# Kernel tuning notes

Hardware: AMD Instinct MI355X
Metric: run time of the kernel (lower is better)

The kernel has to match this reference:

```python
import jax, jax.numpy as jnp
import numpy as np

LN_EPS = 1e-5


def setup_inputs() -> dict:
    key = jax.random.key(0)
    ks = jax.random.split(key, 6)
    B, M, N, D = 16, 128, 128, 128
    NM, H = 16, 512
    xav = float(np.sqrt(2.0 / (D + D)))  # xavier_normal over (in_dim, out_dim) fan
    return {
        "x": jax.random.normal(ks[0], (B, M, N, D), jnp.float32),
        "w1": jax.random.normal(ks[1], (D, D, NM, 2), jnp.float32) * xav,
        "w2": jax.random.normal(ks[2], (D, D, NM, 2), jnp.float32) * xav,
        "ff_w0": jax.random.normal(ks[3], (D, H), jnp.float32) * float(1.0 / np.sqrt(D)),
        "ff_b0": jnp.zeros((H,), jnp.float32),
        "ff_w1": jax.random.normal(ks[4], (H, D), jnp.float32) * float(1.0 / np.sqrt(H)),
        "ff_b1": jnp.zeros((D,), jnp.float32),
        "ln_g": jnp.ones((D,), jnp.float32),
        "ln_b": jnp.zeros((D,), jnp.float32),
    }


def _layer_norm(h, g, b):
    mu = jnp.mean(h, axis=-1, keepdims=True)
    var = jnp.mean(jnp.square(h - mu), axis=-1, keepdims=True)
    return (h - mu) * jax.lax.rsqrt(var + LN_EPS) * g + b


def _forward_fourier(x, w1, w2):
    # x: [B, M, N, I] -> [B, I, M, N]
    xt = jnp.transpose(x, (0, 3, 1, 2))
    B, I, M, N = xt.shape
    nm = w1.shape[2]
    cw1 = w1[..., 0] + 1j * w1[..., 1]  # [I, O, nm]
    cw2 = w2[..., 0] + 1j * w2[..., 1]
    O = cw1.shape[1]

    # Fourier along last axis (y)
    fty = jnp.fft.rfft(xt, axis=-1, norm="ortho")                    # [B,I,M,N//2+1]
    f1 = jnp.einsum("bixy,ioy->boxy", fty[..., :nm], cw1)            # [B,O,M,nm]
    pad_y = jnp.zeros((B, O, M, N // 2 + 1 - nm), dtype=f1.dtype)
    xy = jnp.fft.irfft(jnp.concatenate([f1, pad_y], axis=-1), n=N, axis=-1, norm="ortho")

    # Fourier along second-to-last axis (x)
    ftx = jnp.fft.rfft(xt, axis=-2, norm="ortho")                    # [B,I,M//2+1,N]
    f2 = jnp.einsum("bixy,iox->boxy", ftx[:, :, :nm, :], cw2)        # [B,O,nm,N]
    pad_x = jnp.zeros((B, O, M // 2 + 1 - nm, N), dtype=f2.dtype)
    xx = jnp.fft.irfft(jnp.concatenate([f2, pad_x], axis=-2), n=M, axis=-2, norm="ortho")

    return jnp.transpose(xx + xy, (0, 2, 3, 1))  # [B,M,N,O]


def reference(x, w1, w2, ff_w0, ff_b0, ff_w1, ff_b1, ln_g, ln_b):
    h = _forward_fourier(x, w1, w2)
    # backcast FeedForward: Linear -> ReLU -> Linear -> LayerNorm (dropout=0)
    h1 = jax.nn.relu(jnp.einsum("bmni,ih->bmnh", h, ff_w0) + ff_b0)
    h2 = jnp.einsum("bmnh,ho->bmno", h1, ff_w1) + ff_b1
    return _layer_norm(h2, ln_g, ln_b)
```

## Files before the change

kernel.cpp:

```cpp
#include <hip/hip_runtime.h>


#define LN_EPS 1e-5f
#define NMODES 16
#define FROW 4096
#define HROW 16384

typedef __attribute__((ext_vector_type(8))) short short8;
typedef __attribute__((ext_vector_type(4))) short short4v;
typedef __attribute__((ext_vector_type(4))) float f32x4;

__device__ __forceinline__ ushort f2bf(float f) {
    unsigned u = __float_as_uint(f);
    unsigned r = (u + 0x7FFFu + ((u >> 16) & 1u)) >> 16;
    return (ushort)r;
}
__device__ __forceinline__ float bf2f(ushort h) {
    return __uint_as_float(((unsigned)h) << 16);
}

__global__ void k_setup(float* __restrict__ Tc, float* __restrict__ Ts,
                        float* __restrict__ IT) {
    const float invs = 0.08838834764831845f;
    for (int idx = threadIdx.x; idx < NMODES * 128; idx += blockDim.x) {
        int k = idx >> 7, n = idx & 127;
        int p = (k * n) & 127;
        float th = (float)p * (6.283185307179586f / 128.0f);
        float c = cosf(th), s = sinf(th);
        Tc[idx] = c * invs;
        Ts[idx] = -s * invs;
        float ck = (k == 0) ? invs : 2.0f * invs;
        IT[n * 32 + 2 * k]     = ck * c;
        IT[n * 32 + 2 * k + 1] = -ck * s;
    }
}

__global__ void k_wpack(const float* __restrict__ w, ushort* __restrict__ Wph,
                        ushort* __restrict__ Wpl) {
    int idx = blockIdx.x * 256 + threadIdx.x;
    int k  = idx >> 16;
    int op = (idx >> 8) & 255;
    int ip = idx & 255;
    int i = ip & 127, o = op & 127;
    const float* base = w + (((i << 7) | o) * NMODES + k) * 2;
    float re = base[0], im = base[1];
    float v = (ip < 128) ? ((op < 128) ? re : im)
                         : ((op < 128) ? -im : re);
    ushort hi = f2bf(v);
    ushort lo = f2bf(v - bf2f(hi));
    Wph[idx] = hi;
    Wpl[idx] = lo;
}

__global__ __launch_bounds__(256) void k_wcvt(const float* __restrict__ w0,
        const float* __restrict__ w1, ushort* __restrict__ w0t,
        ushort* __restrict__ w1t) {
    int idx = blockIdx.x * 256 + threadIdx.x;
    int h = idx >> 7, k = idx & 127;
    w0t[idx] = f2bf(w0[k * 512 + h]);
    int o = idx >> 9, hh = idx & 511;
    w1t[idx] = f2bf(w1[hh * 128 + o]);
}

__global__ __launch_bounds__(128) void k_fft(const float* __restrict__ x,
        const float* __restrict__ Tc, const float* __restrict__ Ts,
        float* __restrict__ F, int mode) {
    __shared__ float Tc_s[NMODES * 128];
    __shared__ float Ts_s[NMODES * 128];
    for (int e = threadIdx.x; e < NMODES * 128; e += 128) {
        Tc_s[e] = Tc[e];
        Ts_s[e] = Ts[e];
    }
    __syncthreads();
    int row = blockIdx.x;
    int base, ts;
    if (mode == 0) { base = row * HROW; ts = 128; }
    else { base = (row >> 7) * 2097152 + (row & 127) * 128; ts = 16384; }
    int i = threadIdx.x;
    float re[NMODES], im[NMODES];
#pragma unroll
    for (int k = 0; k < NMODES; ++k) { re[k] = 0.f; im[k] = 0.f; }
    for (int tb = 0; tb < 32; ++tb) {
        int t0 = tb * 4;
        float xv0 = x[base + (t0 + 0) * ts + i];
        float xv1 = x[base + (t0 + 1) * ts + i];
        float xv2 = x[base + (t0 + 2) * ts + i];
        float xv3 = x[base + (t0 + 3) * ts + i];
#pragma unroll
        for (int k = 0; k < NMODES; ++k) {
            f32x4 c4 = *(const f32x4*)&Tc_s[k * 128 + t0];
            f32x4 s4 = *(const f32x4*)&Ts_s[k * 128 + t0];
            re[k] += xv0 * c4[0] + xv1 * c4[1] + xv2 * c4[2] + xv3 * c4[3];
            im[k] += xv0 * s4[0] + xv1 * s4[1] + xv2 * s4[2] + xv3 * s4[3];
        }
    }
    float* outp = F + row * FROW;
#pragma unroll
    for (int k = 0; k < NMODES; ++k) {
        outp[k * 256 + i]       = re[k];
        outp[k * 256 + 128 + i] = im[k];
    }
}

__global__ __launch_bounds__(256) void k_mixm(const float* __restrict__ A,
        const ushort* __restrict__ Wph, const ushort* __restrict__ Wpl,
        float* __restrict__ outF) {
    __shared__ ushort Ah[32 * 264];
    __shared__ ushort Al[32 * 264];
    int tid = threadIdx.x;
    int kt = blockIdx.x & 15;
    int bm0 = (blockIdx.x >> 4) * 32;
    {
        int row = tid >> 3, cg = tid & 7;
        const float* arow = A + (bm0 + row) * FROW + kt * 256 + cg * 32;
        ushort* ah = &Ah[row * 264 + cg * 32];
        ushort* al = &Al[row * 264 + cg * 32];
#pragma unroll
        for (int j = 0; j < 8; ++j) {
            f32x4 v = *(const f32x4*)(arow + j * 4);
            short4v h4, l4;
#pragma unroll
            for (int q = 0; q < 4; ++q) {
                ushort h = f2bf(v[q]);
                h4[q] = (short)h;
                l4[q] = (short)f2bf(v[q] - bf2f(h));
            }
            *(short4v*)(ah + j * 4) = h4;
            *(short4v*)(al + j * 4) = l4;
        }
    }
    __syncthreads();
    int lane = tid & 63, wid = tid >> 6;
    int frow = lane & 15, fk8 = (lane >> 4) * 8, fr4 = (lane >> 4) * 4;
    f32x4 acc[2][4];
#pragma unroll
    for (int a = 0; a < 2; ++a)
#pragma unroll
        for (int c = 0; c < 4; ++c) acc[a][c] = {0.f, 0.f, 0.f, 0.f};
    const ushort* wph = Wph + kt * 65536;
    const ushort* wpl = Wpl + kt * 65536;
#pragma unroll
    for (int kk = 0; kk < 8; ++kk) {
        short8 ah0 = *(const short8*)&Ah[(frow)      * 264 + kk * 32 + fk8];
        short8 ah1 = *(const short8*)&Ah[(16 + frow) * 264 + kk * 32 + fk8];
        short8 al0 = *(const short8*)&Al[(frow)      * 264 + kk * 32 + fk8];
        short8 al1 = *(const short8*)&Al[(16 + frow) * 264 + kk * 32 + fk8];
#pragma unroll
        for (int tc = 0; tc < 4; ++tc) {
            int op = wid * 64 + tc * 16 + frow;
            int base = op * 256 + kk * 32 + fk8;
            short8 wh = *(const short8*)&wph[base];
            short8 wl = *(const short8*)&wpl[base];
            acc[0][tc] = __builtin_amdgcn_mfma_f32_16x16x32_bf16(ah0, wh, acc[0][tc], 0, 0, 0);
            acc[0][tc] = __builtin_amdgcn_mfma_f32_16x16x32_bf16(ah0, wl, acc[0][tc], 0, 0, 0);
            acc[0][tc] = __builtin_amdgcn_mfma_f32_16x16x32_bf16(al0, wh, acc[0][tc], 0, 0, 0);
            acc[1][tc] = __builtin_amdgcn_mfma_f32_16x16x32_bf16(ah1, wh, acc[1][tc], 0, 0, 0);
            acc[1][tc] = __builtin_amdgcn_mfma_f32_16x16x32_bf16(ah1, wl, acc[1][tc], 0, 0, 0);
            acc[1][tc] = __builtin_amdgcn_mfma_f32_16x16x32_bf16(al1, wh, acc[1][tc], 0, 0, 0);
        }
    }
#pragma unroll
    for (int tr = 0; tr < 2; ++tr)
#pragma unroll
        for (int tc = 0; tc < 4; ++tc)
#pragma unroll
            for (int r = 0; r < 4; ++r)
                outF[(bm0 + tr * 16 + fr4 + r) * FROW + kt * 256 + wid * 64 + tc * 16 + frow]
                    = acc[tr][tc][r];
}

__global__ __launch_bounds__(256) void k_icdft(const float* __restrict__ f,
        const float* __restrict__ IT, float* __restrict__ h, int mode) {
    __shared__ float IT_s[128 * 32];
    __shared__ float f_s[32 * 128];
    int row = blockIdx.x;
    for (int e = threadIdx.x; e < 4096; e += 256) {
        IT_s[e] = IT[e];
        f_s[e]  = f[row * FROW + e];
    }
    __syncthreads();
    int o = threadIdx.x & 127, nh = threadIdx.x >> 7;
    int outbase, ostride;
    if (mode == 0) { outbase = row * HROW + o; ostride = 128; }
    else { outbase = (row >> 7) * 2097152 + (row & 127) * 128 + o; ostride = 16384; }
    for (int nb = 0; nb < 8; ++nb) {
        int n0 = nh * 64 + nb * 8;
        float acc[8];
#pragma unroll
        for (int j = 0; j < 8; ++j) acc[j] = 0.f;
#pragma unroll
        for (int kpb = 0; kpb < 8; ++kpb) {
            int kp0 = kpb * 4;
            float f0 = f_s[kp0 * 128 + o];
            float f1v = f_s[kp0 * 128 + 128 + o];
            float f2v = f_s[kp0 * 128 + 256 + o];
            float f3v = f_s[kp0 * 128 + 384 + o];
#pragma unroll
            for (int j = 0; j < 8; ++j) {
                f32x4 it = *(const f32x4*)&IT_s[(n0 + j) * 32 + kp0];
                acc[j] += f0 * it[0] + f1v * it[1] + f2v * it[2] + f3v * it[3];
            }
        }
        if (mode == 0) {
#pragma unroll
            for (int j = 0; j < 8; ++j) h[outbase + (n0 + j) * ostride] = acc[j];
        } else {
#pragma unroll
            for (int j = 0; j < 8; ++j) h[outbase + (n0 + j) * ostride] += acc[j];
        }
    }
}

__global__ __launch_bounds__(256) void k_ffn(float* __restrict__ hio,
        const ushort* __restrict__ w0t, const float* __restrict__ b0,
        const ushort* __restrict__ w1t, const float* __restrict__ b1,
        const float* __restrict__ g, const float* __restrict__ bb) {
    __shared__ __align__(16) ushort h1_s[64 * 136];
    __shared__ float b0_s[512];
    __shared__ float gb_s[256];
    __shared__ float b1_s[128];
    __shared__ float ps_s[64 * 4];
    __shared__ float pq_s[64 * 4];
    __shared__ float mr_s[64 * 2];

    int tid = threadIdx.x;
    int R0 = blockIdx.x * 64;
    for (int e = tid; e < 512; e += 256) b0_s[e] = b0[e];
    if (tid < 128) {
        gb_s[tid] = g[tid];
        gb_s[128 + tid] = bb[tid];
        b1_s[tid] = b1[tid];
    }

    int lane = tid & 63, wid = tid >> 6;
    int frow = lane & 15;
    int fk8 = (lane >> 4) * 8;
    int fr4 = (lane >> 4) * 4;

    short8 a1f[4][4];
#pragma unroll
    for (int tr = 0; tr < 4; ++tr)
#pragma unroll
        for (int kk = 0; kk < 4; ++kk) {
            const float* src = &hio[(R0 + tr * 16 + frow) * 128 + kk * 32 + fk8];
            f32x4 v0 = *(const f32x4*)src;
            f32x4 v1 = *(const f32x4*)(src + 4);
            short8 t;
#pragma unroll
            for (int j = 0; j < 4; ++j) {
                t[j]     = (short)f2bf(v0[j]);
                t[4 + j] = (short)f2bf(v1[j]);
            }
            a1f[tr][kk] = t;
        }

    f32x4 acc2[4][2];
#pragma unroll
    for (int a = 0; a < 4; ++a)
#pragma unroll
        for (int c = 0; c < 2; ++c) acc2[a][c] = {0.f, 0.f, 0.f, 0.f};

    for (int hc = 0; hc < 4; ++hc) {
        __syncthreads();
#pragma unroll
        for (int tc = 0; tc < 2; ++tc) {
            int lcol = wid * 32 + tc * 16 + frow;
            int hcol = hc * 128 + lcol;
            short8 bfr[4];
#pragma unroll
            for (int kk = 0; kk < 4; ++kk)
                bfr[kk] = *(const short8*)&w0t[hcol * 128 + kk * 32 + fk8];
            f32x4 acc1[4];
#pragma unroll
            for (int a = 0; a < 4; ++a) acc1[a] = {0.f, 0.f, 0.f, 0.f};
#pragma unroll
            for (int kk = 0; kk < 4; ++kk)
#pragma unroll
                for (int tr = 0; tr < 4; ++tr)
                    acc1[tr] = __builtin_amdgcn_mfma_f32_16x16x32_bf16(
                        a1f[tr][kk], bfr[kk], acc1[tr], 0, 0, 0);
            float b0v = b0_s[hcol];
#pragma unroll
            for (int tr = 0; tr < 4; ++tr)
#pragma unroll
                for (int r = 0; r < 4; ++r) {
                    float v = acc1[tr][r] + b0v;
                    h1_s[(tr * 16 + fr4 + r) * 136 + lcol] = f2bf(fmaxf(v, 0.f));
                }
        }
        __syncthreads();
#pragma unroll
        for (int kk = 0; kk < 4; ++kk) {
            short8 a2[4];
#pragma unroll
            for (int tr = 0; tr < 4; ++tr)
                a2[tr] = *(const short8*)&h1_s[(tr * 16 + frow) * 136 + kk * 32 + fk8];
#pragma unroll
            for (int tc = 0; tc < 2; ++tc) {
                int ocol = wid * 32 + tc * 16 + frow;
                short8 b2 = *(const short8*)&w1t[ocol * 512 + hc * 128 + kk * 32 + fk8];
#pragma unroll
                for (int tr = 0; tr < 4; ++tr)
                    acc2[tr][tc] = __builtin_amdgcn_mfma_f32_16x16x32_bf16(
                        a2[tr], b2, acc2[tr][tc], 0, 0, 0);
            }
        }
    }
    float b1v0 = b1_s[wid * 32 + frow];
    float b1v1 = b1_s[wid * 32 + 16 + frow];
#pragma unroll
    for (int tr = 0; tr < 4; ++tr)
#pragma unroll
        for (int r = 0; r < 4; ++r) {
            float v0 = acc2[tr][0][r] + b1v0;
            float v1 = acc2[tr][1][r] + b1v1;
            acc2[tr][0][r] = v0;
            acc2[tr][1][r] = v1;
            float s = v0 + v1;
            float q = v0 * v0 + v1 * v1;
            s += __shfl_xor(s, 1); q += __shfl_xor(q, 1);
            s += __shfl_xor(s, 2); q += __shfl_xor(q, 2);
            s += __shfl_xor(s, 4); q += __shfl_xor(q, 4);
            s += __shfl_xor(s, 8); q += __shfl_xor(q, 8);
            if (frow == 0) {
                int row_l = tr * 16 + fr4 + r;
                ps_s[row_l * 4 + wid] = s;
                pq_s[row_l * 4 + wid] = q;
            }
        }
    __syncthreads();
    if (tid < 64) {
        float S = ps_s[tid * 4] + ps_s[tid * 4 + 1] + ps_s[tid * 4 + 2] + ps_s[tid * 4 + 3];
        float Q = pq_s[tid * 4] + pq_s[tid * 4 + 1] + pq_s[tid * 4 + 2] + pq_s[tid * 4 + 3];
        float mu = S * (1.0f / 128.0f);
        float var = Q * (1.0f / 128.0f) - mu * mu;
        mr_s[tid * 2] = mu;
        mr_s[tid * 2 + 1] = rsqrtf(fmaxf(var, 0.f) + LN_EPS);
    }
    __syncthreads();
    float g0 = gb_s[wid * 32 + frow],       bb0 = gb_s[128 + wid * 32 + frow];
    float g1 = gb_s[wid * 32 + 16 + frow],  bb1 = gb_s[128 + wid * 32 + 16 + frow];
#pragma unroll
    for (int tr = 0; tr < 4; ++tr)
#pragma unroll
        for (int r = 0; r < 4; ++r) {
            int row_l = tr * 16 + fr4 + r;
            float mu = mr_s[row_l * 2], rs = mr_s[row_l * 2 + 1];
            float* orow = &hio[(R0 + row_l) * 128 + wid * 32];
            orow[frow]      = (acc2[tr][0][r] - mu) * rs * g0 + bb0;
            orow[16 + frow] = (acc2[tr][1][r] - mu) * rs * g1 + bb1;
        }
}

extern "C" void kernel_launch(void* const* d_in, const int* in_sizes, int n_in,
                              void* d_out, int out_size, void* d_ws, size_t ws_size,
                              hipStream_t stream) {
    (void)in_sizes; (void)n_in; (void)out_size; (void)ws_size;
    const float* x   = (const float*)d_in[0];
    const float* w1  = (const float*)d_in[1];
    const float* w2  = (const float*)d_in[2];
    const float* fw0 = (const float*)d_in[3];
    const float* fb0 = (const float*)d_in[4];
    const float* fw1 = (const float*)d_in[5];
    const float* fb1 = (const float*)d_in[6];
    const float* lng = (const float*)d_in[7];
    const float* lnb = (const float*)d_in[8];
    float* out = (float*)d_out;

    char* ws = (char*)d_ws;
    float*  Tc  = (float*)(ws);
    float*  Ts  = (float*)(ws + 8192);
    float*  IT  = (float*)(ws + 16384);
    ushort* Wph = (ushort*)(ws + 32768);
    ushort* Wpl = (ushort*)(ws + 32768 + 2097152);
    ushort* w0t = (ushort*)(ws + 4227072);
    ushort* w1t = (ushort*)(ws + 4358144);
    float*  buf0 = (float*)(ws + 4489216);
    float*  buf1 = (float*)(ws + 4489216 + 33554432);

    k_setup<<<1, 256, 0, stream>>>(Tc, Ts, IT);
    k_wcvt <<<256, 256, 0, stream>>>(fw0, fw1, w0t, w1t);

    k_wpack<<<4096, 256, 0, stream>>>(w1, Wph, Wpl);
    k_fft  <<<2048, 128, 0, stream>>>(x, Tc, Ts, buf0, 0);
    k_mixm <<<1024, 256, 0, stream>>>(buf0, Wph, Wpl, buf1);
    k_icdft<<<2048, 256, 0, stream>>>(buf1, IT, out, 0);

    k_wpack<<<4096, 256, 0, stream>>>(w2, Wph, Wpl);
    k_fft  <<<2048, 128, 0, stream>>>(x, Tc, Ts, buf0, 1);
    k_mixm <<<1024, 256, 0, stream>>>(buf0, Wph, Wpl, buf1);
    k_icdft<<<2048, 256, 0, stream>>>(buf1, IT, out, 1);

    k_ffn<<<4096, 256, 0, stream>>>(out, w0t, fb0, w1t, fb1, lng, lnb);
}
```

Baseline: 564.0 us.

## Emit bf16 intermediate from inverse DFT and stage FFN tiles through LDS

The second inverse-DFT pass now writes the summed spectral output as bf16 into a separate workspace buffer when the workspace is large enough, halving the bytes the FFN kernel reads. The FFN kernel loads its input tile cooperatively into LDS with coalesced vector loads instead of per-lane strided register fragments. It also stages the LayerNorm output through LDS for coalesced vector stores. This trades higher LDS usage (lower occupancy risk) and a gated path that depends on workspace size for less global traffic and better coalescing.

```diff
diff --git a/kernel.cpp b/kernel.cpp
--- a/kernel.cpp
+++ b/kernel.cpp
@@ -7,6 +7,7 @@
 #define HROW 16384
 
 typedef __attribute__((ext_vector_type(8))) short short8;
+typedef __attribute__((ext_vector_type(8))) ushort ushort8;
 typedef __attribute__((ext_vector_type(4))) short short4v;
 typedef __attribute__((ext_vector_type(4))) float f32x4;
 
@@ -170,7 +171,8 @@
 }
 
 __global__ __launch_bounds__(256) void k_icdft(const float* __restrict__ f,
-        const float* __restrict__ IT, float* __restrict__ h, int mode) {
+        const float* __restrict__ IT, float* __restrict__ h,
+        ushort* __restrict__ hbf, int mode, int use_bf) {
     __shared__ float IT_s[128 * 32];
     __shared__ float f_s[32 * 128];
     int row = blockIdx.x;
@@ -204,6 +206,12 @@
         if (mode == 0) {
 #pragma unroll
             for (int j = 0; j < 8; ++j) h[outbase + (n0 + j) * ostride] = acc[j];
+        } else if (use_bf) {
+#pragma unroll
+            for (int j = 0; j < 8; ++j) {
+                int ix = outbase + (n0 + j) * ostride;
+                hbf[ix] = f2bf(h[ix] + acc[j]);
+            }
         } else {
 #pragma unroll
             for (int j = 0; j < 8; ++j) h[outbase + (n0 + j) * ostride] += acc[j];
@@ -211,48 +219,49 @@
     }
 }
 
-__global__ __launch_bounds__(256) void k_ffn(float* __restrict__ hio,
+__global__ __launch_bounds__(256) void k_ffn(const ushort* __restrict__ hbf,
+        const float* __restrict__ h32, float* __restrict__ out,
         const ushort* __restrict__ w0t, const float* __restrict__ b0,
         const ushort* __restrict__ w1t, const float* __restrict__ b1,
-        const float* __restrict__ g, const float* __restrict__ bb) {
-    __shared__ __align__(16) ushort h1_s[64 * 136];
-    __shared__ float b0_s[512];
+        const float* __restrict__ g, const float* __restrict__ bb, int use_bf) {
+    __shared__ __align__(16) char smem[34816];
+    ushort* h_s  = (ushort*)smem;
+    ushort* h1_s = (ushort*)(smem + 17408);
+    float*  h2f  = (float*)smem;
+    float*  ps_s = (float*)(smem + 33792);
+    __shared__ float b0q_s[512];
     __shared__ float gb_s[256];
     __shared__ float b1_s[128];
-    __shared__ float ps_s[64 * 4];
-    __shared__ float pq_s[64 * 4];
-    __shared__ float mr_s[64 * 2];
+    __shared__ float mr_s[128];
 
     int tid = threadIdx.x;
     int R0 = blockIdx.x * 64;
-    for (int e = tid; e < 512; e += 256) b0_s[e] = b0[e];
-    if (tid < 128) {
-        gb_s[tid] = g[tid];
-        gb_s[128 + tid] = bb[tid];
-        b1_s[tid] = b1[tid];
-    }
+    {
+        int srow = tid >> 2, scol = (tid & 3) * 32;
+        if (use_bf) {
+            const ushort* src = hbf + (R0 + srow) * 128 + scol;
+#pragma unroll
+            for (int j = 0; j < 4; ++j)
+                *(ushort8*)&h_s[srow * 136 + scol + j * 8] = *(const ushort8*)(src + j * 8);
+        } else {
+            const float* src = h32 + (R0 + srow) * 128 + scol;
+#pragma unroll
+            for (int j = 0; j < 4; ++j) {
+                f32x4 v0 = *(const f32x4*)(src + j * 8);
+                f32x4 v1 = *(const f32x4*)(src + j * 8 + 4);
+                ushort8 t;
+#pragma unroll
+                for (int q = 0; q < 4; ++q) { t[q] = f2bf(v0[q]); t[4 + q] = f2bf(v1[q]); }
+                *(ushort8*)&h_s[srow * 136 + scol + j * 8] = t;
+            }
+        }
+    }
+    for (int e = tid; e < 512; e += 256) b0q_s[e] = b0[e];
+    if (tid < 128) { gb_s[tid] = g[tid]; gb_s[128 + tid] = bb[tid]; b1_s[tid] = b1[tid]; }
+    __syncthreads();
 
     int lane = tid & 63, wid = tid >> 6;
-    int frow = lane & 15;
-    int fk8 = (lane >> 4) * 8;
-    int fr4 = (lane >> 4) * 4;
-
-    short8 a1f[4][4];
-#pragma unroll
-    for (int tr = 0; tr < 4; ++tr)
-#pragma unroll
-        for (int kk = 0; kk < 4; ++kk) {
-            const float* src = &hio[(R0 + tr * 16 + frow) * 128 + kk * 32 + fk8];
-            f32x4 v0 = *(const f32x4*)src;
-            f32x4 v1 = *(const f32x4*)(src + 4);
-            short8 t;
-#pragma unroll
-            for (int j = 0; j < 4; ++j) {
-                t[j]     = (short)f2bf(v0[j]);
-                t[4 + j] = (short)f2bf(v1[j]);
-            }
-            a1f[tr][kk] = t;
-        }
+    int frow = lane & 15, fk8 = (lane >> 4) * 8, fr4 = (lane >> 4) * 4;
 
     f32x4 acc2[4][2];
 #pragma unroll
@@ -261,7 +270,6 @@
         for (int c = 0; c < 2; ++c) acc2[a][c] = {0.f, 0.f, 0.f, 0.f};
 
     for (int hc = 0; hc < 4; ++hc) {
-        __syncthreads();
 #pragma unroll
         for (int tc = 0; tc < 2; ++tc) {
             int lcol = wid * 32 + tc * 16 + frow;
@@ -276,10 +284,12 @@
 #pragma unroll
             for (int kk = 0; kk < 4; ++kk)
 #pragma unroll
-                for (int tr = 0; tr < 4; ++tr)
+                for (int tr = 0; tr < 4; ++tr) {
+                    short8 av = *(const short8*)&h_s[(tr * 16 + frow) * 136 + kk * 32 + fk8];
                     acc1[tr] = __builtin_amdgcn_mfma_f32_16x16x32_bf16(
-                        a1f[tr][kk], bfr[kk], acc1[tr], 0, 0, 0);
-            float b0v = b0_s[hcol];
+                        av, bfr[kk], acc1[tr], 0, 0, 0);
+                }
+            float b0v = b0q_s[hcol];
 #pragma unroll
             for (int tr = 0; tr < 4; ++tr)
 #pragma unroll
@@ -290,22 +300,25 @@
         }
         __syncthreads();
 #pragma unroll
-        for (int kk = 0; kk < 4; ++kk) {
-            short8 a2[4];
-#pragma unroll
-            for (int tr = 0; tr < 4; ++tr)
-                a2[tr] = *(const short8*)&h1_s[(tr * 16 + frow) * 136 + kk * 32 + fk8];
-#pragma unroll
-            for (int tc = 0; tc < 2; ++tc) {
-                int ocol = wid * 32 + tc * 16 + frow;
-                short8 b2 = *(const short8*)&w1t[ocol * 512 + hc * 128 + kk * 32 + fk8];
-#pragma unroll
-                for (int tr = 0; tr < 4; ++tr)
+        for (int tc = 0; tc < 2; ++tc) {
+            int ocol = wid * 32 + tc * 16 + frow;
+            short8 b2f[4];
+#pragma unroll
+            for (int kk = 0; kk < 4; ++kk)
+                b2f[kk] = *(const short8*)&w1t[ocol * 512 + hc * 128 + kk * 32 + fk8];
+#pragma unroll
+            for (int kk = 0; kk < 4; ++kk)
+#pragma unroll
+                for (int tr = 0; tr < 4; ++tr) {
+                    short8 a2 = *(const short8*)&h1_s[(tr * 16 + frow) * 136 + kk * 32 + fk8];
                     acc2[tr][tc] = __builtin_amdgcn_mfma_f32_16x16x32_bf16(
-                        a2[tr], b2, acc2[tr][tc], 0, 0, 0);
-            }
-        }
-    }
+                        a2, b2f[kk], acc2[tr][tc], 0, 0, 0);
+                }
+        }
+        __syncthreads();
+    }
+
+    float* pq_s = b0q_s;
     float b1v0 = b1_s[wid * 32 + frow];
     float b1v1 = b1_s[wid * 32 + 16 + frow];
 #pragma unroll
@@ -334,28 +347,35 @@
         float Q = pq_s[tid * 4] + pq_s[tid * 4 + 1] + pq_s[tid * 4 + 2] + pq_s[tid * 4 + 3];
         float mu = S * (1.0f / 128.0f);
         float var = Q * (1.0f / 128.0f) - mu * mu;
-        mr_s[tid * 2] = mu;
-        mr_s[tid * 2 + 1] = rsqrtf(fmaxf(var, 0.f) + LN_EPS);
-    }
-    __syncthreads();
-    float g0 = gb_s[wid * 32 + frow],       bb0 = gb_s[128 + wid * 32 + frow];
-    float g1 = gb_s[wid * 32 + 16 + frow],  bb1 = gb_s[128 + wid * 32 + 16 + frow];
+        mr_s[tid] = mu;
+        mr_s[64 + tid] = rsqrtf(fmaxf(var, 0.f) + LN_EPS);
+    }
+    __syncthreads();
+    float g0 = gb_s[wid * 32 + frow],      c0 = gb_s[128 + wid * 32 + frow];
+    float g1 = gb_s[wid * 32 + 16 + frow], c1 = gb_s[128 + wid * 32 + 16 + frow];
 #pragma unroll
     for (int tr = 0; tr < 4; ++tr)
 #pragma unroll
         for (int r = 0; r < 4; ++r) {
             int row_l = tr * 16 + fr4 + r;
-            float mu = mr_s[row_l * 2], rs = mr_s[row_l * 2 + 1];
-            float* orow = &hio[(R0 + row_l) * 128 + wid * 32];
-            orow[frow]      = (acc2[tr][0][r] - mu) * rs * g0 + bb0;
-            orow[16 + frow] = (acc2[tr][1][r] - mu) * rs * g1 + bb1;
-        }
+            float mu = mr_s[row_l], rs = mr_s[64 + row_l];
+            h2f[row_l * 132 + wid * 32 + frow]      = (acc2[tr][0][r] - mu) * rs * g0 + c0;
+            h2f[row_l * 132 + wid * 32 + 16 + frow] = (acc2[tr][1][r] - mu) * rs * g1 + c1;
+        }
+    __syncthreads();
+    {
+        int srow = tid >> 2, scol = (tid & 3) * 32;
+        float* dst = out + (R0 + srow) * 128 + scol;
+#pragma unroll
+        for (int j = 0; j < 8; ++j)
+            *(f32x4*)(dst + j * 4) = *(const f32x4*)&h2f[srow * 132 + scol + j * 4];
+    }
 }
 
 extern "C" void kernel_launch(void* const* d_in, const int* in_sizes, int n_in,
                               void* d_out, int out_size, void* d_ws, size_t ws_size,
                               hipStream_t stream) {
-    (void)in_sizes; (void)n_in; (void)out_size; (void)ws_size;
+    (void)in_sizes; (void)n_in; (void)out_size;
     const float* x   = (const float*)d_in[0];
     const float* w1  = (const float*)d_in[1];
     const float* w2  = (const float*)d_in[2];
@@ -377,6 +397,9 @@
     ushort* w1t = (ushort*)(ws + 4358144);
     float*  buf0 = (float*)(ws + 4489216);
     float*  buf1 = (float*)(ws + 4489216 + 33554432);
+    ushort* hbf  = (ushort*)(ws + 71598080);
+    const size_t need = 71598080ull + 67108864ull;
+    int use_bf = (ws_size >= need) ? 1 : 0;
 
     k_setup<<<1, 256, 0, stream>>>(Tc, Ts, IT);
     k_wcvt <<<256, 256, 0, stream>>>(fw0, fw1, w0t, w1t);
@@ -384,12 +407,12 @@
     k_wpack<<<4096, 256, 0, stream>>>(w1, Wph, Wpl);
     k_fft  <<<2048, 128, 0, stream>>>(x, Tc, Ts, buf0, 0);
     k_mixm <<<1024, 256, 0, stream>>>(buf0, Wph, Wpl, buf1);
-    k_icdft<<<2048, 256, 0, stream>>>(buf1, IT, out, 0);
+    k_icdft<<<2048, 256, 0, stream>>>(buf1, IT, out, hbf, 0, use_bf);
 
     k_wpack<<<4096, 256, 0, stream>>>(w2, Wph, Wpl);
     k_fft  <<<2048, 128, 0, stream>>>(x, Tc, Ts, buf0, 1);
     k_mixm <<<1024, 256, 0, stream>>>(buf0, Wph, Wpl, buf1);
-    k_icdft<<<2048, 256, 0, stream>>>(buf1, IT, out, 1);
-
-    k_ffn<<<4096, 256, 0, stream>>>(out, w0t, fb0, w1t, fb1, lng, lnb);
-}
+    k_icdft<<<2048, 256, 0, stream>>>(buf1, IT, out, hbf, 1, use_bf);
+
+    k_ffn<<<4096, 256, 0, stream>>>(hbf, out, out, w0t, fb0, w1t, fb1, lng, lnb, use_bf);
+}
```

Result: faster. 531.3 us (-5.8%).

## Store Fourier branch outputs as bf16 and fuse their sum into FFN

Applied to the files above, without the earlier changes.

The inverse DFT now writes each branch's output as bf16 into separate contiguous buffers, avoiding the strided fp32 read-modify-write accumulation into the output. The FFN kernel reads both bf16 buffers, adds them in shared memory and applies the full FFN plus LayerNorm, using one wave per 64-row block that holds all 128 output columns. This lets LayerNorm finish within a wave without block-level reductions or extra barriers. It also runs k_mixm in place on buf0, and falls back to an fp32 path when the workspace is too small. The risks are extra bf16 rounding of the branch outputs and heavier register pressure in the single-wave FFN.

```diff
diff --git a/kernel.cpp b/kernel.cpp
--- a/kernel.cpp
+++ b/kernel.cpp
@@ -7,6 +7,7 @@
 #define HROW 16384
 
 typedef __attribute__((ext_vector_type(8))) short short8;
+typedef __attribute__((ext_vector_type(8))) ushort ushort8;
 typedef __attribute__((ext_vector_type(4))) short short4v;
 typedef __attribute__((ext_vector_type(4))) float f32x4;
 
@@ -170,7 +171,8 @@
 }
 
 __global__ __launch_bounds__(256) void k_icdft(const float* __restrict__ f,
-        const float* __restrict__ IT, float* __restrict__ h, int mode) {
+        const float* __restrict__ IT, ushort* __restrict__ obf,
+        float* __restrict__ h32, ushort* __restrict__ hbfs, int mode) {
     __shared__ float IT_s[128 * 32];
     __shared__ float f_s[32 * 128];
     int row = blockIdx.x;
@@ -180,9 +182,6 @@
     }
     __syncthreads();
     int o = threadIdx.x & 127, nh = threadIdx.x >> 7;
-    int outbase, ostride;
-    if (mode == 0) { outbase = row * HROW + o; ostride = 128; }
-    else { outbase = (row >> 7) * 2097152 + (row & 127) * 128 + o; ostride = 16384; }
     for (int nb = 0; nb < 8; ++nb) {
         int n0 = nh * 64 + nb * 8;
         float acc[8];
@@ -203,159 +202,145 @@
         }
         if (mode == 0) {
 #pragma unroll
-            for (int j = 0; j < 8; ++j) h[outbase + (n0 + j) * ostride] = acc[j];
+            for (int j = 0; j < 8; ++j)
+                obf[row * HROW + (n0 + j) * 128 + o] = f2bf(acc[j]);
+        } else if (mode == 1) {
+#pragma unroll
+            for (int j = 0; j < 8; ++j)
+                h32[row * HROW + (n0 + j) * 128 + o] = acc[j];
         } else {
 #pragma unroll
-            for (int j = 0; j < 8; ++j) h[outbase + (n0 + j) * ostride] += acc[j];
-        }
-    }
-}
-
-__global__ __launch_bounds__(256) void k_ffn(float* __restrict__ hio,
+            for (int j = 0; j < 8; ++j) {
+                int ix = (row >> 7) * 2097152 + (row & 127) * 128 + o + (n0 + j) * 16384;
+                hbfs[ix] = f2bf(h32[ix] + acc[j]);
+            }
+        }
+    }
+}
+
+__global__ __launch_bounds__(64, 2) void k_ffn(const ushort* __restrict__ hy,
+        const ushort* __restrict__ hx, const ushort* __restrict__ hbfs,
+        float* __restrict__ out,
         const ushort* __restrict__ w0t, const float* __restrict__ b0,
         const ushort* __restrict__ w1t, const float* __restrict__ b1,
-        const float* __restrict__ g, const float* __restrict__ bb) {
-    __shared__ __align__(16) ushort h1_s[64 * 136];
-    __shared__ float b0_s[512];
-    __shared__ float gb_s[256];
-    __shared__ float b1_s[128];
-    __shared__ float ps_s[64 * 4];
-    __shared__ float pq_s[64 * 4];
-    __shared__ float mr_s[64 * 2];
-
-    int tid = threadIdx.x;
+        const float* __restrict__ g, const float* __restrict__ bb, int two) {
+    __shared__ __align__(16) ushort h_s[64 * 136];
+    __shared__ __align__(16) ushort h1_s[64 * 40];
+    int lane = threadIdx.x;
     int R0 = blockIdx.x * 64;
-    for (int e = tid; e < 512; e += 256) b0_s[e] = b0[e];
-    if (tid < 128) {
-        gb_s[tid] = g[tid];
-        gb_s[128 + tid] = bb[tid];
-        b1_s[tid] = b1[tid];
-    }
-
-    int lane = tid & 63, wid = tid >> 6;
-    int frow = lane & 15;
-    int fk8 = (lane >> 4) * 8;
-    int fr4 = (lane >> 4) * 4;
-
-    short8 a1f[4][4];
+
+    if (two) {
+        int b = R0 >> 14, m = (R0 >> 7) & 127, n0 = R0 & 127;
+        const ushort* hyp = hy + (size_t)R0 * 128;
+        const ushort* hxp = hx + (size_t)b * 2097152 + (size_t)n0 * 16384 + m * 128;
+        for (int e = lane; e < 1024; e += 64) {
+            int rl = e >> 4, c8 = (e & 15) * 8;
+            ushort8 a = *(const ushort8*)&hyp[rl * 128 + c8];
+            ushort8 c = *(const ushort8*)&hxp[rl * 16384 + c8];
+            ushort8 t;
+#pragma unroll
+            for (int j = 0; j < 8; ++j) t[j] = f2bf(bf2f(a[j]) + bf2f(c[j]));
+            *(ushort8*)&h_s[rl * 136 + c8] = t;
+        }
+    } else {
+        for (int e = lane; e < 1024; e += 64) {
+            int rl = e >> 4, c8 = (e & 15) * 8;
+            *(ushort8*)&h_s[rl * 136 + c8] =
+                *(const ushort8*)&hbfs[(size_t)(R0 + rl) * 128 + c8];
+        }
+    }
+    __syncthreads();
+
+    int frow = lane & 15, qg = lane >> 4;
+    int fk8 = qg * 8, fr4 = qg * 4;
+
+    f32x4 acc2[4][8];
+#pragma unroll
+    for (int a = 0; a < 4; ++a)
+#pragma unroll
+        for (int c = 0; c < 8; ++c) acc2[a][c] = {0.f, 0.f, 0.f, 0.f};
+
+    for (int ch = 0; ch < 16; ++ch) {
+        short8 bfr[2][4];
+#pragma unroll
+        for (int tc2 = 0; tc2 < 2; ++tc2)
+#pragma unroll
+            for (int kk = 0; kk < 4; ++kk)
+                bfr[tc2][kk] = *(const short8*)&w0t[(ch * 32 + tc2 * 16 + frow) * 128 + kk * 32 + fk8];
+        f32x4 acc1[4][2];
+#pragma unroll
+        for (int a = 0; a < 4; ++a)
+#pragma unroll
+            for (int c = 0; c < 2; ++c) acc1[a][c] = {0.f, 0.f, 0.f, 0.f};
+#pragma unroll
+        for (int kk = 0; kk < 4; ++kk)
+#pragma unroll
+            for (int tr = 0; tr < 4; ++tr) {
+                short8 av = *(const short8*)&h_s[(tr * 16 + frow) * 136 + kk * 32 + fk8];
+#pragma unroll
+                for (int tc2 = 0; tc2 < 2; ++tc2)
+                    acc1[tr][tc2] = __builtin_amdgcn_mfma_f32_16x16x32_bf16(
+                        av, bfr[tc2][kk], acc1[tr][tc2], 0, 0, 0);
+            }
+#pragma unroll
+        for (int tc2 = 0; tc2 < 2; ++tc2) {
+            float b0v = b0[ch * 32 + tc2 * 16 + frow];
+#pragma unroll
+            for (int tr = 0; tr < 4; ++tr)
+#pragma unroll
+                for (int r = 0; r < 4; ++r)
+                    h1_s[(tr * 16 + fr4 + r) * 40 + tc2 * 16 + frow] =
+                        f2bf(fmaxf(acc1[tr][tc2][r] + b0v, 0.f));
+        }
+        short8 b2[8];
+#pragma unroll
+        for (int tc = 0; tc < 8; ++tc)
+            b2[tc] = *(const short8*)&w1t[(tc * 16 + frow) * 512 + ch * 32 + fk8];
+#pragma unroll
+        for (int tr = 0; tr < 4; ++tr) {
+            short8 a2 = *(const short8*)&h1_s[(tr * 16 + frow) * 40 + fk8];
+#pragma unroll
+            for (int tc = 0; tc < 8; ++tc)
+                acc2[tr][tc] = __builtin_amdgcn_mfma_f32_16x16x32_bf16(
+                    a2, b2[tc], acc2[tr][tc], 0, 0, 0);
+        }
+    }
+
+    float b1v[8], gv[8], bv[8];
+#pragma unroll
+    for (int tc = 0; tc < 8; ++tc) {
+        int o = tc * 16 + frow;
+        b1v[tc] = b1[o]; gv[tc] = g[o]; bv[tc] = bb[o];
+    }
 #pragma unroll
     for (int tr = 0; tr < 4; ++tr)
 #pragma unroll
-        for (int kk = 0; kk < 4; ++kk) {
-            const float* src = &hio[(R0 + tr * 16 + frow) * 128 + kk * 32 + fk8];
-            f32x4 v0 = *(const f32x4*)src;
-            f32x4 v1 = *(const f32x4*)(src + 4);
-            short8 t;
-#pragma unroll
-            for (int j = 0; j < 4; ++j) {
-                t[j]     = (short)f2bf(v0[j]);
-                t[4 + j] = (short)f2bf(v1[j]);
-            }
-            a1f[tr][kk] = t;
-        }
-
-    f32x4 acc2[4][2];
-#pragma unroll
-    for (int a = 0; a < 4; ++a)
-#pragma unroll
-        for (int c = 0; c < 2; ++c) acc2[a][c] = {0.f, 0.f, 0.f, 0.f};
-
-    for (int hc = 0; hc < 4; ++hc) {
-        __syncthreads();
-#pragma unroll
-        for (int tc = 0; tc < 2; ++tc) {
-            int lcol = wid * 32 + tc * 16 + frow;
-            int hcol = hc * 128 + lcol;
-            short8 bfr[4];
-#pragma unroll
-            for (int kk = 0; kk < 4; ++kk)
-                bfr[kk] = *(const short8*)&w0t[hcol * 128 + kk * 32 + fk8];
-            f32x4 acc1[4];
-#pragma unroll
-            for (int a = 0; a < 4; ++a) acc1[a] = {0.f, 0.f, 0.f, 0.f};
-#pragma unroll
-            for (int kk = 0; kk < 4; ++kk)
-#pragma unroll
-                for (int tr = 0; tr < 4; ++tr)
-                    acc1[tr] = __builtin_amdgcn_mfma_f32_16x16x32_bf16(
-                        a1f[tr][kk], bfr[kk], acc1[tr], 0, 0, 0);
-            float b0v = b0_s[hcol];
-#pragma unroll
-            for (int tr = 0; tr < 4; ++tr)
-#pragma unroll
-                for (int r = 0; r < 4; ++r) {
-                    float v = acc1[tr][r] + b0v;
-                    h1_s[(tr * 16 + fr4 + r) * 136 + lcol] = f2bf(fmaxf(v, 0.f));
-                }
-        }
-        __syncthreads();
-#pragma unroll
-        for (int kk = 0; kk < 4; ++kk) {
-            short8 a2[4];
-#pragma unroll
-            for (int tr = 0; tr < 4; ++tr)
-                a2[tr] = *(const short8*)&h1_s[(tr * 16 + frow) * 136 + kk * 32 + fk8];
-#pragma unroll
-            for (int tc = 0; tc < 2; ++tc) {
-                int ocol = wid * 32 + tc * 16 + frow;
-                short8 b2 = *(const short8*)&w1t[ocol * 512 + hc * 128 + kk * 32 + fk8];
-#pragma unroll
-                for (int tr = 0; tr < 4; ++tr)
-                    acc2[tr][tc] = __builtin_amdgcn_mfma_f32_16x16x32_bf16(
-                        a2[tr], b2, acc2[tr][tc], 0, 0, 0);
-            }
-        }
-    }
-    float b1v0 = b1_s[wid * 32 + frow];
-    float b1v1 = b1_s[wid * 32 + 16 + frow];
-#pragma unroll
-    for (int tr = 0; tr < 4; ++tr)
-#pragma unroll
         for (int r = 0; r < 4; ++r) {
-            float v0 = acc2[tr][0][r] + b1v0;
-            float v1 = acc2[tr][1][r] + b1v1;
-            acc2[tr][0][r] = v0;
-            acc2[tr][1][r] = v1;
-            float s = v0 + v1;
-            float q = v0 * v0 + v1 * v1;
-            s += __shfl_xor(s, 1); q += __shfl_xor(q, 1);
-            s += __shfl_xor(s, 2); q += __shfl_xor(q, 2);
-            s += __shfl_xor(s, 4); q += __shfl_xor(q, 4);
-            s += __shfl_xor(s, 8); q += __shfl_xor(q, 8);
-            if (frow == 0) {
-                int row_l = tr * 16 + fr4 + r;
-                ps_s[row_l * 4 + wid] = s;
-                pq_s[row_l * 4 + wid] = q;
-            }
-        }
-    __syncthreads();
-    if (tid < 64) {
-        float S = ps_s[tid * 4] + ps_s[tid * 4 + 1] + ps_s[tid * 4 + 2] + ps_s[tid * 4 + 3];
-        float Q = pq_s[tid * 4] + pq_s[tid * 4 + 1] + pq_s[tid * 4 + 2] + pq_s[tid * 4 + 3];
-        float mu = S * (1.0f / 128.0f);
-        float var = Q * (1.0f / 128.0f) - mu * mu;
-        mr_s[tid * 2] = mu;
-        mr_s[tid * 2 + 1] = rsqrtf(fmaxf(var, 0.f) + LN_EPS);
-    }
-    __syncthreads();
-    float g0 = gb_s[wid * 32 + frow],       bb0 = gb_s[128 + wid * 32 + frow];
-    float g1 = gb_s[wid * 32 + 16 + frow],  bb1 = gb_s[128 + wid * 32 + 16 + frow];
-#pragma unroll
-    for (int tr = 0; tr < 4; ++tr)
-#pragma unroll
-        for (int r = 0; r < 4; ++r) {
-            int row_l = tr * 16 + fr4 + r;
-            float mu = mr_s[row_l * 2], rs = mr_s[row_l * 2 + 1];
-            float* orow = &hio[(R0 + row_l) * 128 + wid * 32];
-            orow[frow]      = (acc2[tr][0][r] - mu) * rs * g0 + bb0;
-            orow[16 + frow] = (acc2[tr][1][r] - mu) * rs * g1 + bb1;
+            float s = 0.f, qq = 0.f;
+#pragma unroll
+            for (int tc = 0; tc < 8; ++tc) {
+                float v = acc2[tr][tc][r] + b1v[tc];
+                acc2[tr][tc][r] = v;
+                s += v; qq += v * v;
+            }
+            s += __shfl_xor(s, 1); qq += __shfl_xor(qq, 1);
+            s += __shfl_xor(s, 2); qq += __shfl_xor(qq, 2);
+            s += __shfl_xor(s, 4); qq += __shfl_xor(qq, 4);
+            s += __shfl_xor(s, 8); qq += __shfl_xor(qq, 8);
+            float mu = s * (1.0f / 128.0f);
+            float var = qq * (1.0f / 128.0f) - mu * mu;
+            float rs = rsqrtf(fmaxf(var, 0.f) + LN_EPS);
+            float* orow = &out[(size_t)(R0 + tr * 16 + fr4 + r) * 128];
+#pragma unroll
+            for (int tc = 0; tc < 8; ++tc)
+                orow[tc * 16 + frow] = (acc2[tr][tc][r] - mu) * rs * gv[tc] + bv[tc];
         }
 }
 
 extern "C" void kernel_launch(void* const* d_in, const int* in_sizes, int n_in,
                               void* d_out, int out_size, void* d_ws, size_t ws_size,
                               hipStream_t stream) {
-    (void)in_sizes; (void)n_in; (void)out_size; (void)ws_size;
+    (void)in_sizes; (void)n_in; (void)out_size;
     const float* x   = (const float*)d_in[0];
     const float* w1  = (const float*)d_in[1];
     const float* w2  = (const float*)d_in[2];
@@ -376,20 +361,26 @@
     ushort* w0t = (ushort*)(ws + 4227072);
     ushort* w1t = (ushort*)(ws + 4358144);
     float*  buf0 = (float*)(ws + 4489216);
-    float*  buf1 = (float*)(ws + 4489216 + 33554432);
+    ushort* hy   = (ushort*)(ws + 38043648);
+    ushort* hx   = (ushort*)(ws + 105152512);
+    const size_t need_two = 172261376ull;
+    int two = (ws_size >= need_two) ? 1 : 0;
+    ushort* hbfs = hy;
 
     k_setup<<<1, 256, 0, stream>>>(Tc, Ts, IT);
     k_wcvt <<<256, 256, 0, stream>>>(fw0, fw1, w0t, w1t);
 
     k_wpack<<<4096, 256, 0, stream>>>(w1, Wph, Wpl);
     k_fft  <<<2048, 128, 0, stream>>>(x, Tc, Ts, buf0, 0);
-    k_mixm <<<1024, 256, 0, stream>>>(buf0, Wph, Wpl, buf1);
-    k_icdft<<<2048, 256, 0, stream>>>(buf1, IT, out, 0);
+    k_mixm <<<1024, 256, 0, stream>>>(buf0, Wph, Wpl, buf0);
+    if (two) k_icdft<<<2048, 256, 0, stream>>>(buf0, IT, hy, out, hbfs, 0);
+    else     k_icdft<<<2048, 256, 0, stream>>>(buf0, IT, hy, out, hbfs, 1);
 
     k_wpack<<<4096, 256, 0, stream>>>(w2, Wph, Wpl);
     k_fft  <<<2048, 128, 0, stream>>>(x, Tc, Ts, buf0, 1);
-    k_mixm <<<1024, 256, 0, stream>>>(buf0, Wph, Wpl, buf1);
-    k_icdft<<<2048, 256, 0, stream>>>(buf1, IT, out, 1);
-
-    k_ffn<<<4096, 256, 0, stream>>>(out, w0t, fb0, w1t, fb1, lng, lnb);
-}
+    k_mixm <<<1024, 256, 0, stream>>>(buf0, Wph, Wpl, buf0);
+    if (two) k_icdft<<<2048, 256, 0, stream>>>(buf0, IT, hx, out, hbfs, 0);
+    else     k_icdft<<<2048, 256, 0, stream>>>(buf0, IT, hx, out, hbfs, 2);
+
+    k_ffn<<<4096, 64, 0, stream>>>(hy, hx, hbfs, out, w0t, fb0, w1t, fb1, lng, lnb, two);
+}
```

New measurement: 522.5 us. 1.08x faster.
